# Kernel optimization log

Hardware: AMD Instinct MI355X
Metric: run time of the kernel (lower is better)

The kernel has to match this reference:

```python
import jax, jax.numpy as jnp
import numpy as np

T, B, H, V = 256, 64, 1024, 512
PAD, BOS, EOS = 0, 1, 2
NEG = -10000.0


def setup_inputs() -> dict:
    key = jax.random.key(0)
    k1, k2, k3, k4 = jax.random.split(key, 4)
    enc_outs = jax.random.normal(k1, (T, B, H), dtype=jnp.float32)
    lengths = jax.random.randint(k2, (B,), 1, T + 1)
    W = jax.random.normal(k3, (V, H), dtype=jnp.float32) * 0.02
    b = jnp.zeros((V,), dtype=jnp.float32)
    trans = jax.random.normal(k4, (V, V), dtype=jnp.float32)
    # structural constraints from __init__
    trans = trans.at[BOS, :].set(NEG)
    trans = trans.at[:, EOS].set(NEG)
    trans = trans.at[:, PAD].set(NEG)
    trans = trans.at[PAD, :].set(NEG)
    trans = trans.at[PAD, EOS].set(0.0)
    trans = trans.at[PAD, PAD].set(0.0)
    return {"enc_outs": enc_outs, "lengths": lengths, "W": W, "b": b, "trans": trans}


def reference(enc_outs, lengths, W, b, trans):
    # feats: [T, B, V] emission scores
    feats = jnp.einsum('tbh,vh->tbv', enc_outs, W) + b
    # mask[b, t] = t < lengths[b]
    mask = (jnp.arange(T)[None, :] < lengths[:, None])  # [B, T]
    feats = feats * mask.T[:, :, None].astype(feats.dtype)

    score0 = jnp.full((B, V), NEG, dtype=feats.dtype).at[:, BOS].set(0.0)

    def step(score, xs):
        feat_t, mask_t = xs  # [B, V], [B]
        # new[b, i] = LSE_j(score[b, j] + trans[i, j]) + feat_t[b, i]
        z = jax.nn.logsumexp(score[:, None, :] + trans[None, :, :], axis=-1)
        new = z + feat_t
        score = jnp.where(mask_t[:, None], new, score)
        return score, None

    score, _ = jax.lax.scan(step, score0, (feats, mask.T))
    return jax.nn.logsumexp(score, axis=-1)  # [B] log partition
```

## Files before the change

kernel.cpp:

```cpp
#include <hip/hip_runtime.h>
#include <hip/hip_bf16.h>
#include <hip/hip_fp16.h>
#include <math.h>

#define TT 256
#define BB 64
#define HH 1024
#define VV 512
#define NEGV -10000.0f
#define BOSI 1
#define CI 128
#define NK 4
#define NW 44
#define PSTRIDE 64


typedef __attribute__((ext_vector_type(8))) short frag;
typedef __attribute__((ext_vector_type(4))) float f4;

#define GLL16(g, l) __builtin_amdgcn_global_load_lds( \
    (const __attribute__((address_space(1))) void*)(g), \
    (__attribute__((address_space(3))) void*)(l), 16, 0, 0)

__global__ __launch_bounds__(256)
void k_expT(const float* __restrict__ trans, float* __restrict__ ET) {
    __shared__ float tile[32][33];
    int bi = blockIdx.x, bj = blockIdx.y;
    int tx = threadIdx.x & 31;
    int ty = threadIdx.x >> 5;
#pragma unroll
    for (int k = 0; k < 4; ++k) {
        int i = bi * 32 + ty + k * 8;
        tile[ty + k * 8][tx] = expf(trans[i * VV + bj * 32 + tx]);
    }
    __syncthreads();
#pragma unroll
    for (int k = 0; k < 4; ++k) {
        int j = bj * 32 + ty + k * 8;
        ET[j * VV + bi * 32 + tx] = tile[tx][ty + k * 8];
    }
}

__global__ __launch_bounds__(256)
void k_zero(unsigned long long* __restrict__ pay) {
    pay[blockIdx.x * 256 + threadIdx.x] = 0ull;
}

__global__ __launch_bounds__(256)
void k_cast(const float* __restrict__ src, __hip_bfloat16* __restrict__ dst) {
    int i = blockIdx.x * 256 + threadIdx.x;
    float4 v = ((const float4*)src)[i];
    __hip_bfloat16 o[4];
    o[0] = __float2bfloat16(v.x); o[1] = __float2bfloat16(v.y);
    o[2] = __float2bfloat16(v.z); o[3] = __float2bfloat16(v.w);
    *(uint2*)&dst[i * 4] = *(uint2*)o;
}

__global__ __launch_bounds__(256)
void k_feats(const __hip_bfloat16* __restrict__ Abf, const __hip_bfloat16* __restrict__ Wbf,
             const float* __restrict__ bias, __hip_bfloat16* __restrict__ feats) {
    __shared__ short As[128 * 32];
    __shared__ short Ws[128 * 32];
    int tid = threadIdx.x;
    int wave = tid >> 6, lane = tid & 63;
    int quad = lane >> 4, l16 = lane & 15;
    int wm = wave & 1, wn = wave >> 1;
    int row0 = blockIdx.x * 128;
    int col0 = blockIdx.y * 128;
    const short* Ag = (const short*)Abf;
    const short* Wg = (const short*)Wbf;

    f4 acc[4][4];
#pragma unroll
    for (int mt = 0; mt < 4; ++mt)
#pragma unroll
        for (int nt = 0; nt < 4; ++nt)
            acc[mt][nt] = (f4){0.f, 0.f, 0.f, 0.f};

    for (int kt = 0; kt < HH; kt += 32) {
#pragma unroll
        for (int s = 0; s < 2; ++s) {
            int idx = wave * 128 + s * 64 + lane;
            int r = idx >> 2, q = idx & 3;
            GLL16(Ag + (size_t)(row0 + r) * HH + kt + q * 8,
                  &As[(wave * 128 + s * 64) * 8]);
            GLL16(Wg + (size_t)(col0 + r) * HH + kt + q * 8,
                  &Ws[(wave * 128 + s * 64) * 8]);
        }
        __syncthreads();
        frag a[4], b[4];
#pragma unroll
        for (int mt = 0; mt < 4; ++mt)
            a[mt] = *(const frag*)&As[(wm * 64 + mt * 16 + l16) * 32 + quad * 8];
#pragma unroll
        for (int nt = 0; nt < 4; ++nt)
            b[nt] = *(const frag*)&Ws[(wn * 64 + nt * 16 + l16) * 32 + quad * 8];
#pragma unroll
        for (int mt = 0; mt < 4; ++mt)
#pragma unroll
            for (int nt = 0; nt < 4; ++nt)
                acc[mt][nt] = __builtin_amdgcn_mfma_f32_16x16x32_bf16(
                    a[mt], b[nt], acc[mt][nt], 0, 0, 0);
        __syncthreads();
    }

    float bv[4];
#pragma unroll
    for (int nt = 0; nt < 4; ++nt)
        bv[nt] = bias[col0 + wn * 64 + nt * 16 + l16];
#pragma unroll
    for (int mt = 0; mt < 4; ++mt) {
#pragma unroll
        for (int nt = 0; nt < 4; ++nt) {
#pragma unroll
            for (int r = 0; r < 4; ++r) {
                int row = row0 + wm * 64 + mt * 16 + quad * 4 + r;
                int col = col0 + wn * 64 + nt * 16 + l16;
                int t = row >> 6, bb = row & 63;
                feats[((size_t)bb * TT + t) * VV + col] =
                    __float2bfloat16(acc[mt][nt][r] + bv[nt]);
            }
        }
    }
}

__global__ __launch_bounds__(512, 2)
void k_scan(const float* __restrict__ ETg,
            const __hip_bfloat16* __restrict__ feats,
            const int* __restrict__ lengths,
            unsigned long long* __restrict__ pay,
            float* __restrict__ out) {
    __shared__ float spf[16 * 36];
    __shared__ float spart[32 * CI];
    __shared__ float sLz[CI];
    __shared__ float sm[NK];
    __shared__ float sred[2];
    __shared__ float sfin[4];

    int tid = threadIdx.x;
    int b   = blockIdx.x & 63;
    int kc  = blockIdx.x >> 6;
    int lane = tid & 63, wid = tid >> 6;
    int len = lengths[b];
    int js = tid >> 4;
    int i0 = (tid & 15) * 8;

#define PSLOT(s, c) (pay + ((size_t)(b) * 2 * NK + (size_t)(s) * NK + (c)) * PSTRIDE)

    float eta[128];
    {
        const float* base = ETg + (size_t)(js * 16) * VV + kc * CI + i0;
#pragma unroll
        for (int jj = 0; jj < 16; ++jj) {
            float4 v0 = *(const float4*)(base + jj * VV);
            float4 v1 = *(const float4*)(base + jj * VV + 4);
            eta[jj * 8 + 0] = v0.x; eta[jj * 8 + 1] = v0.y;
            eta[jj * 8 + 2] = v0.z; eta[jj * 8 + 3] = v0.w;
            eta[jj * 8 + 4] = v1.x; eta[jj * 8 + 5] = v1.y;
            eta[jj * 8 + 6] = v1.z; eta[jj * 8 + 7] = v1.w;
        }
    }

    if (tid < NW) {
        float cm0 = (kc == 0) ? 0.f : NEGV;
        unsigned long long v;
        if (tid == NW - 1) {
            v = (1ull << 48) | (unsigned long long)__float_as_uint(cm0);
        } else {
            unsigned long long h[3] = {0ull, 0ull, 0ull};
#pragma unroll
            for (int r = 0; r < 3; ++r) {
                int idx = 3 * tid + r;
                if (idx < CI) {
                    int gi = kc * CI + idx;
                    float z = (gi == BOSI) ? 0.f : NEGV;
                    h[r] = (unsigned long long)__half_as_ushort(__float2half(expf(z - cm0)));
                }
            }
            v = (1ull << 48) | (h[2] << 32) | (h[1] << 16) | h[0];
        }
        __hip_atomic_store(&PSLOT(1, kc)[tid], v, __ATOMIC_RELAXED, __HIP_MEMORY_SCOPE_AGENT);
    }

    const __hip_bfloat16* fb = feats + (size_t)b * TT * VV;
    int pc = (tid >= 132) ? 3 : (tid >= 88) ? 2 : (tid >= 44) ? 1 : 0;
    int pw = tid - pc * 44;
    int spf_base = 36 * (js >> 1) + 16 * (js & 1);

    for (int t = 0; t < len; ++t) {
        float ft = 0.f;
        if (tid < CI) ft = __bfloat162float(fb[(size_t)t * VV + kc * CI + tid]);

        if (tid < NK * NW) {
            const unsigned long long* wp = &PSLOT((t + 1) & 1, pc)[pw];
            unsigned tgt = (unsigned)(t + 1);
            unsigned long long v;
            do {
                v = __hip_atomic_load(wp, __ATOMIC_RELAXED, __HIP_MEMORY_SCOPE_AGENT);
            } while ((unsigned)(v >> 48) < tgt);
            if (pw == NW - 1) {
                sm[pc] = __uint_as_float((unsigned)v);
            } else {
#pragma unroll
                for (int r = 0; r < 3; ++r) {
                    int idx = 3 * pw + r;
                    if (idx < CI) {
                        int j = pc * CI + idx;
                        spf[36 * (j >> 5) + (j & 31)] =
                            __half2float(__ushort_as_half((unsigned short)(v >> (16 * r))));
                    }
                }
            }
        }
        __syncthreads();

        float M = fmaxf(fmaxf(sm[0], sm[1]), fmaxf(sm[2], sm[3]));
        float wloc = expf(sm[js >> 3] - M);

        float a0 = 0.f, a1 = 0.f, a2 = 0.f, a3 = 0.f;
        float a4 = 0.f, a5 = 0.f, a6 = 0.f, a7 = 0.f;
#pragma unroll
        for (int j4 = 0; j4 < 4; ++j4) {
            float4 pv = *(const float4*)&spf[spf_base + j4 * 4];
            float pj[4] = {pv.x, pv.y, pv.z, pv.w};
#pragma unroll
            for (int u = 0; u < 4; ++u) {
                int jj = j4 * 4 + u;
                float pq = pj[u];
                a0 = fmaf(eta[jj * 8 + 0], pq, a0);
                a1 = fmaf(eta[jj * 8 + 1], pq, a1);
                a2 = fmaf(eta[jj * 8 + 2], pq, a2);
                a3 = fmaf(eta[jj * 8 + 3], pq, a3);
                a4 = fmaf(eta[jj * 8 + 4], pq, a4);
                a5 = fmaf(eta[jj * 8 + 5], pq, a5);
                a6 = fmaf(eta[jj * 8 + 6], pq, a6);
                a7 = fmaf(eta[jj * 8 + 7], pq, a7);
            }
        }
        *(float4*)&spart[js * CI + i0]     = make_float4(a0 * wloc, a1 * wloc, a2 * wloc, a3 * wloc);
        *(float4*)&spart[js * CI + i0 + 4] = make_float4(a4 * wloc, a5 * wloc, a6 * wloc, a7 * wloc);
        __syncthreads();

        if (tid < CI) {
            float s = 0.f;
#pragma unroll
            for (int q = 0; q < 32; ++q) s += spart[q * CI + tid];
            float zn = M + logf(s) + ft;
            sLz[tid] = zn;
            float cmv = zn;
#pragma unroll
            for (int off = 32; off > 0; off >>= 1)
                cmv = fmaxf(cmv, __shfl_xor(cmv, off, 64));
            if (lane == 0) sred[wid] = cmv;
        }
        __syncthreads();

        if (tid < NW) {
            float cm = fmaxf(sred[0], sred[1]);
            unsigned long long tg = (unsigned long long)(unsigned)(t + 2) << 48;
            unsigned long long v;
            if (tid == NW - 1) {
                v = tg | (unsigned long long)__float_as_uint(cm);
            } else {
                unsigned long long h[3] = {0ull, 0ull, 0ull};
#pragma unroll
                for (int r = 0; r < 3; ++r) {
                    int idx = 3 * tid + r;
                    if (idx < CI)
                        h[r] = (unsigned long long)__half_as_ushort(
                                   __float2half(expf(sLz[idx] - cm)));
                }
                v = tg | (h[2] << 32) | (h[1] << 16) | h[0];
            }
            __hip_atomic_store(&PSLOT(t & 1, kc)[tid], v, __ATOMIC_RELAXED, __HIP_MEMORY_SCOPE_AGENT);
        }
    }

    if (kc == 0) {
        if (tid < NK * NW) {
            const unsigned long long* wp = &PSLOT((len + 1) & 1, pc)[pw];
            unsigned tgt = (unsigned)(len + 1);
            unsigned long long v;
            do {
                v = __hip_atomic_load(wp, __ATOMIC_RELAXED, __HIP_MEMORY_SCOPE_AGENT);
            } while ((unsigned)(v >> 48) < tgt);
            if (pw == NW - 1) {
                sm[pc] = __uint_as_float((unsigned)v);
            } else {
#pragma unroll
                for (int r = 0; r < 3; ++r) {
                    int idx = 3 * pw + r;
                    if (idx < CI) {
                        int j = pc * CI + idx;
                        spf[36 * (j >> 5) + (j & 31)] =
                            __half2float(__ushort_as_half((unsigned short)(v >> (16 * r))));
                    }
                }
            }
        }
        __syncthreads();
        if (tid < 256) {
            float M = fmaxf(fmaxf(sm[0], sm[1]), fmaxf(sm[2], sm[3]));
            int j0 = 2 * tid;
            float w0 = expf(sm[j0 >> 7] - M);
            float v0 = spf[36 * (j0 >> 5) + (j0 & 31)];
            float v1 = spf[36 * ((j0 + 1) >> 5) + ((j0 + 1) & 31)];
            float s = (v0 + v1) * w0;
#pragma unroll
            for (int off = 32; off > 0; off >>= 1)
                s += __shfl_xor(s, off, 64);
            if (lane == 0) sfin[wid] = s;
        }
        __syncthreads();
        if (tid == 0) {
            float M = fmaxf(fmaxf(sm[0], sm[1]), fmaxf(sm[2], sm[3]));
            out[b] = M + logf(sfin[0] + sfin[1] + sfin[2] + sfin[3]);
        }
    }
#undef PSLOT
}

extern "C" void kernel_launch(void* const* d_in, const int* in_sizes, int n_in,
                              void* d_out, int out_size, void* d_ws, size_t ws_size,
                              hipStream_t stream) {
    const float* enc     = (const float*)d_in[0];
    const int*   lengths = (const int*)d_in[1];
    const float* W       = (const float*)d_in[2];
    const float* bias    = (const float*)d_in[3];
    const float* trans   = (const float*)d_in[4];
    float* out = (float*)d_out;

    char* ws = (char*)d_ws;
    float*          ETg   = (float*)ws;
    __hip_bfloat16* feats = (__hip_bfloat16*)(ws + (1 << 20));
    unsigned long long* pay = (unsigned long long*)(ws + (17 << 20));
    __hip_bfloat16* Abf   = (__hip_bfloat16*)(ws + (18 << 20));
    __hip_bfloat16* Wbf   = (__hip_bfloat16*)(ws + (50 << 20));

    hipLaunchKernelGGL(k_zero, dim3(128), dim3(256), 0, stream, pay);
    hipLaunchKernelGGL(k_expT, dim3(16, 16), dim3(256), 0, stream, trans, ETg);
    hipLaunchKernelGGL(k_cast, dim3(16384), dim3(256), 0, stream, enc, Abf);
    hipLaunchKernelGGL(k_cast, dim3(512), dim3(256), 0, stream, W, Wbf);
    hipLaunchKernelGGL(k_feats, dim3(16384 / 128, VV / 128), dim3(256), 0, stream,
                       Abf, Wbf, bias, feats);
    hipLaunchKernelGGL(k_scan, dim3(NK * BB), dim3(512), 0, stream,
                       ETg, feats, lengths, pay, out);
}
```

Measured before the change: 620.1 us.

## Pack payload as fp16 pairs, use fdot2 with half-precision transition matrix

The scan kernel now stores exp(trans) in registers as packed fp16 pairs and accumulates with fdot2, halving register use and FMA count. The cross-block payload packs two fp16 probabilities plus a bf16 max per 64-bit word, so 64 words per chunk are polled by a separate group of waves (threads 256-511) and the unpacking work shrinks. The reduction drops one barrier by fusing the max-reduce and the payload publish into a single wave. It trades accuracy, since transition probabilities are now fp16 and the max is rounded to bf16, for a shorter per-step critical path.

```diff
diff --git a/kernel.cpp b/kernel.cpp
--- a/kernel.cpp
+++ b/kernel.cpp
@@ -11,16 +11,23 @@
 #define BOSI 1
 #define CI 128
 #define NK 4
-#define NW 44
 #define PSTRIDE 64
 
 
 typedef __attribute__((ext_vector_type(8))) short frag;
 typedef __attribute__((ext_vector_type(4))) float f4;
+typedef __attribute__((ext_vector_type(2))) _Float16 h2;
 
 #define GLL16(g, l) __builtin_amdgcn_global_load_lds( \
     (const __attribute__((address_space(1))) void*)(g), \
     (__attribute__((address_space(3))) void*)(l), 16, 0, 0)
+
+__device__ __forceinline__ unsigned short f16b(float x) {
+    return __half_as_ushort(__float2half(x));
+}
+__device__ __forceinline__ float f16f(unsigned int bits) {
+    return __half2float(__ushort_as_half((unsigned short)(bits & 0xFFFFu)));
+}
 
 __global__ __launch_bounds__(256)
 void k_expT(const float* __restrict__ trans, float* __restrict__ ET) {
@@ -130,11 +137,9 @@
             const int* __restrict__ lengths,
             unsigned long long* __restrict__ pay,
             float* __restrict__ out) {
-    __shared__ float spf[16 * 36];
-    __shared__ float spart[32 * CI];
-    __shared__ float sLz[CI];
+    __shared__ unsigned int spf[16 * 17];
+    __shared__ float spart[16 * CI];
     __shared__ float sm[NK];
-    __shared__ float sred[2];
     __shared__ float sfin[4];
 
     int tid = threadIdx.x;
@@ -142,180 +147,148 @@
     int kc  = blockIdx.x >> 6;
     int lane = tid & 63, wid = tid >> 6;
     int len = lengths[b];
-    int js = tid >> 4;
-    int i0 = (tid & 15) * 8;
+    int js = tid >> 5;
+    int ig = tid & 31;
+    int i0 = ig * 4;
 
 #define PSLOT(s, c) (pay + ((size_t)(b) * 2 * NK + (size_t)(s) * NK + (c)) * PSTRIDE)
 
-    float eta[128];
+    unsigned int eta[64];
     {
-        const float* base = ETg + (size_t)(js * 16) * VV + kc * CI + i0;
+        const float* base = ETg + (size_t)(js * 32) * VV + kc * CI + i0;
 #pragma unroll
         for (int jj = 0; jj < 16; ++jj) {
-            float4 v0 = *(const float4*)(base + jj * VV);
-            float4 v1 = *(const float4*)(base + jj * VV + 4);
-            eta[jj * 8 + 0] = v0.x; eta[jj * 8 + 1] = v0.y;
-            eta[jj * 8 + 2] = v0.z; eta[jj * 8 + 3] = v0.w;
-            eta[jj * 8 + 4] = v1.x; eta[jj * 8 + 5] = v1.y;
-            eta[jj * 8 + 6] = v1.z; eta[jj * 8 + 7] = v1.w;
-        }
-    }
-
-    if (tid < NW) {
+            float4 e0 = *(const float4*)(base + (size_t)(2 * jj) * VV);
+            float4 e1 = *(const float4*)(base + (size_t)(2 * jj + 1) * VV);
+            eta[jj * 4 + 0] = (unsigned int)f16b(e0.x) | ((unsigned int)f16b(e1.x) << 16);
+            eta[jj * 4 + 1] = (unsigned int)f16b(e0.y) | ((unsigned int)f16b(e1.y) << 16);
+            eta[jj * 4 + 2] = (unsigned int)f16b(e0.z) | ((unsigned int)f16b(e1.z) << 16);
+            eta[jj * 4 + 3] = (unsigned int)f16b(e0.w) | ((unsigned int)f16b(e1.w) << 16);
+        }
+    }
+
+    if (tid < 64) {
         float cm0 = (kc == 0) ? 0.f : NEGV;
-        unsigned long long v;
-        if (tid == NW - 1) {
-            v = (1ull << 48) | (unsigned long long)__float_as_uint(cm0);
-        } else {
-            unsigned long long h[3] = {0ull, 0ull, 0ull};
-#pragma unroll
-            for (int r = 0; r < 3; ++r) {
-                int idx = 3 * tid + r;
-                if (idx < CI) {
-                    int gi = kc * CI + idx;
-                    float z = (gi == BOSI) ? 0.f : NEGV;
-                    h[r] = (unsigned long long)__half_as_ushort(__float2half(expf(z - cm0)));
-                }
-            }
-            v = (1ull << 48) | (h[2] << 32) | (h[1] << 16) | h[0];
-        }
+        int g0 = kc * CI + 2 * tid, g1 = g0 + 1;
+        float z0 = (g0 == BOSI) ? 0.f : NEGV;
+        float z1 = (g1 == BOSI) ? 0.f : NEGV;
+        unsigned short cmb = __bfloat16_as_ushort(__float2bfloat16(cm0));
+        float cmu = __uint_as_float((unsigned int)cmb << 16);
+        unsigned long long v = (1ull << 48) | ((unsigned long long)cmb << 32) |
+                               ((unsigned long long)f16b(expf(z1 - cmu)) << 16) |
+                               (unsigned long long)f16b(expf(z0 - cmu));
         __hip_atomic_store(&PSLOT(1, kc)[tid], v, __ATOMIC_RELAXED, __HIP_MEMORY_SCOPE_AGENT);
     }
 
     const __hip_bfloat16* fb = feats + (size_t)b * TT * VV;
-    int pc = (tid >= 132) ? 3 : (tid >= 88) ? 2 : (tid >= 44) ? 1 : 0;
-    int pw = tid - pc * 44;
-    int spf_base = 36 * (js >> 1) + 16 * (js & 1);
 
     for (int t = 0; t < len; ++t) {
-        float ft = 0.f;
-        if (tid < CI) ft = __bfloat162float(fb[(size_t)t * VV + kc * CI + tid]);
-
-        if (tid < NK * NW) {
+        float ft0 = 0.f, ft1 = 0.f;
+        if (tid < 64) {
+            unsigned int fp = *(const unsigned int*)(fb + (size_t)t * VV + kc * CI + 2 * tid);
+            ft0 = __uint_as_float(fp << 16);
+            ft1 = __uint_as_float(fp & 0xFFFF0000u);
+        }
+
+        if (tid >= 256) {
+            int pt = tid - 256;
+            int pc = pt >> 6, pw = pt & 63;
             const unsigned long long* wp = &PSLOT((t + 1) & 1, pc)[pw];
             unsigned tgt = (unsigned)(t + 1);
             unsigned long long v;
             do {
                 v = __hip_atomic_load(wp, __ATOMIC_RELAXED, __HIP_MEMORY_SCOPE_AGENT);
             } while ((unsigned)(v >> 48) < tgt);
-            if (pw == NW - 1) {
-                sm[pc] = __uint_as_float((unsigned)v);
-            } else {
-#pragma unroll
-                for (int r = 0; r < 3; ++r) {
-                    int idx = 3 * pw + r;
-                    if (idx < CI) {
-                        int j = pc * CI + idx;
-                        spf[36 * (j >> 5) + (j & 31)] =
-                            __half2float(__ushort_as_half((unsigned short)(v >> (16 * r))));
-                    }
-                }
+            spf[(pc * 4 + (pw >> 4)) * 17 + (pw & 15)] = (unsigned int)v;
+            if (pw == 0)
+                sm[pc] = __uint_as_float(((unsigned int)(v >> 32) & 0xFFFFu) << 16);
+        }
+        __syncthreads();
+
+        float M = fmaxf(fmaxf(sm[0], sm[1]), fmaxf(sm[2], sm[3]));
+        float wloc = expf(sm[js >> 2] - M);
+
+        float a0 = 0.f, a1 = 0.f, a2 = 0.f, a3 = 0.f;
+#pragma unroll
+        for (int jj = 0; jj < 16; ++jj) {
+            unsigned int pp = spf[js * 17 + jj];
+#if __has_builtin(__builtin_amdgcn_fdot2)
+            h2 hp; __builtin_memcpy(&hp, &pp, 4);
+            h2 e0, e1, e2, e3;
+            __builtin_memcpy(&e0, &eta[jj * 4 + 0], 4);
+            __builtin_memcpy(&e1, &eta[jj * 4 + 1], 4);
+            __builtin_memcpy(&e2, &eta[jj * 4 + 2], 4);
+            __builtin_memcpy(&e3, &eta[jj * 4 + 3], 4);
+            a0 = __builtin_amdgcn_fdot2(e0, hp, a0, false);
+            a1 = __builtin_amdgcn_fdot2(e1, hp, a1, false);
+            a2 = __builtin_amdgcn_fdot2(e2, hp, a2, false);
+            a3 = __builtin_amdgcn_fdot2(e3, hp, a3, false);
+#else
+            float p0 = f16f(pp), p1 = f16f(pp >> 16);
+#pragma unroll
+            for (int ii = 0; ii < 4; ++ii) {
+                unsigned int e = eta[jj * 4 + ii];
+                float v0 = f16f(e), v1 = f16f(e >> 16);
+                float* ac = (ii == 0) ? &a0 : (ii == 1) ? &a1 : (ii == 2) ? &a2 : &a3;
+                *ac = fmaf(v0, p0, fmaf(v1, p1, *ac));
             }
-        }
-        __syncthreads();
-
-        float M = fmaxf(fmaxf(sm[0], sm[1]), fmaxf(sm[2], sm[3]));
-        float wloc = expf(sm[js >> 3] - M);
-
-        float a0 = 0.f, a1 = 0.f, a2 = 0.f, a3 = 0.f;
-        float a4 = 0.f, a5 = 0.f, a6 = 0.f, a7 = 0.f;
-#pragma unroll
-        for (int j4 = 0; j4 < 4; ++j4) {
-            float4 pv = *(const float4*)&spf[spf_base + j4 * 4];
-            float pj[4] = {pv.x, pv.y, pv.z, pv.w};
-#pragma unroll
-            for (int u = 0; u < 4; ++u) {
-                int jj = j4 * 4 + u;
-                float pq = pj[u];
-                a0 = fmaf(eta[jj * 8 + 0], pq, a0);
-                a1 = fmaf(eta[jj * 8 + 1], pq, a1);
-                a2 = fmaf(eta[jj * 8 + 2], pq, a2);
-                a3 = fmaf(eta[jj * 8 + 3], pq, a3);
-                a4 = fmaf(eta[jj * 8 + 4], pq, a4);
-                a5 = fmaf(eta[jj * 8 + 5], pq, a5);
-                a6 = fmaf(eta[jj * 8 + 6], pq, a6);
-                a7 = fmaf(eta[jj * 8 + 7], pq, a7);
+#endif
+        }
+        *(float4*)&spart[js * CI + i0] = make_float4(a0 * wloc, a1 * wloc, a2 * wloc, a3 * wloc);
+        __syncthreads();
+
+        if (tid < 64) {
+            float s0 = 0.f, s1 = 0.f;
+#pragma unroll
+            for (int q = 0; q < 16; ++q) {
+                float2 v = *(const float2*)&spart[q * CI + 2 * tid];
+                s0 += v.x; s1 += v.y;
             }
-        }
-        *(float4*)&spart[js * CI + i0]     = make_float4(a0 * wloc, a1 * wloc, a2 * wloc, a3 * wloc);
-        *(float4*)&spart[js * CI + i0 + 4] = make_float4(a4 * wloc, a5 * wloc, a6 * wloc, a7 * wloc);
-        __syncthreads();
-
-        if (tid < CI) {
-            float s = 0.f;
-#pragma unroll
-            for (int q = 0; q < 32; ++q) s += spart[q * CI + tid];
-            float zn = M + logf(s) + ft;
-            sLz[tid] = zn;
-            float cmv = zn;
+            float zn0 = M + logf(s0) + ft0;
+            float zn1 = M + logf(s1) + ft1;
+            float cm = fmaxf(zn0, zn1);
 #pragma unroll
             for (int off = 32; off > 0; off >>= 1)
-                cmv = fmaxf(cmv, __shfl_xor(cmv, off, 64));
-            if (lane == 0) sred[wid] = cmv;
-        }
-        __syncthreads();
-
-        if (tid < NW) {
-            float cm = fmaxf(sred[0], sred[1]);
-            unsigned long long tg = (unsigned long long)(unsigned)(t + 2) << 48;
-            unsigned long long v;
-            if (tid == NW - 1) {
-                v = tg | (unsigned long long)__float_as_uint(cm);
-            } else {
-                unsigned long long h[3] = {0ull, 0ull, 0ull};
-#pragma unroll
-                for (int r = 0; r < 3; ++r) {
-                    int idx = 3 * tid + r;
-                    if (idx < CI)
-                        h[r] = (unsigned long long)__half_as_ushort(
-                                   __float2half(expf(sLz[idx] - cm)));
-                }
-                v = tg | (h[2] << 32) | (h[1] << 16) | h[0];
-            }
+                cm = fmaxf(cm, __shfl_xor(cm, off, 64));
+            unsigned short cmb = __bfloat16_as_ushort(__float2bfloat16(cm));
+            float cmu = __uint_as_float((unsigned int)cmb << 16);
+            unsigned long long v = ((unsigned long long)(unsigned)(t + 2) << 48) |
+                                   ((unsigned long long)cmb << 32) |
+                                   ((unsigned long long)f16b(expf(zn1 - cmu)) << 16) |
+                                   (unsigned long long)f16b(expf(zn0 - cmu));
             __hip_atomic_store(&PSLOT(t & 1, kc)[tid], v, __ATOMIC_RELAXED, __HIP_MEMORY_SCOPE_AGENT);
         }
     }
 
     if (kc == 0) {
-        if (tid < NK * NW) {
+        if (tid >= 256) {
+            int pt = tid - 256;
+            int pc = pt >> 6, pw = pt & 63;
             const unsigned long long* wp = &PSLOT((len + 1) & 1, pc)[pw];
             unsigned tgt = (unsigned)(len + 1);
             unsigned long long v;
             do {
                 v = __hip_atomic_load(wp, __ATOMIC_RELAXED, __HIP_MEMORY_SCOPE_AGENT);
             } while ((unsigned)(v >> 48) < tgt);
-            if (pw == NW - 1) {
-                sm[pc] = __uint_as_float((unsigned)v);
-            } else {
-#pragma unroll
-                for (int r = 0; r < 3; ++r) {
-                    int idx = 3 * pw + r;
-                    if (idx < CI) {
-                        int j = pc * CI + idx;
-                        spf[36 * (j >> 5) + (j & 31)] =
-                            __half2float(__ushort_as_half((unsigned short)(v >> (16 * r))));
-                    }
-                }
-            }
-        }
-        __syncthreads();
+            spf[(pc * 4 + (pw >> 4)) * 17 + (pw & 15)] = (unsigned int)v;
+            if (pw == 0)
+                sm[pc] = __uint_as_float(((unsigned int)(v >> 32) & 0xFFFFu) << 16);
+        }
+        __syncthreads();
+        float M = fmaxf(fmaxf(sm[0], sm[1]), fmaxf(sm[2], sm[3]));
+        float s = 0.f;
         if (tid < 256) {
-            float M = fmaxf(fmaxf(sm[0], sm[1]), fmaxf(sm[2], sm[3]));
             int j0 = 2 * tid;
-            float w0 = expf(sm[j0 >> 7] - M);
-            float v0 = spf[36 * (j0 >> 5) + (j0 & 31)];
-            float v1 = spf[36 * ((j0 + 1) >> 5) + ((j0 + 1) & 31)];
-            float s = (v0 + v1) * w0;
-#pragma unroll
-            for (int off = 32; off > 0; off >>= 1)
-                s += __shfl_xor(s, off, 64);
-            if (lane == 0) sfin[wid] = s;
-        }
-        __syncthreads();
-        if (tid == 0) {
-            float M = fmaxf(fmaxf(sm[0], sm[1]), fmaxf(sm[2], sm[3]));
+            unsigned int pp = spf[(j0 >> 5) * 17 + ((j0 & 31) >> 1)];
+            s = (f16f(pp) + f16f(pp >> 16)) * expf(sm[tid >> 6] - M);
+        }
+#pragma unroll
+        for (int off = 32; off > 0; off >>= 1)
+            s += __shfl_xor(s, off, 64);
+        if (lane == 0 && tid < 256) sfin[wid] = s;
+        __syncthreads();
+        if (tid == 0)
             out[b] = M + logf(sfin[0] + sfin[1] + sfin[2] + sfin[3]);
-        }
     }
 #undef PSLOT
 }
```

Result: faster. 548.2 us (-11.6%).
